# Performance work log

Measured on AMD Instinct MI355X. Metric: run time of the kernel, lower is better.

The kernel has to match this reference:

```python
import jax, jax.numpy as jnp
import numpy as np

N = 100000   # nodes
E = 1600000  # edges (avg degree 16)
D = 128      # in_features == out_features
THETA = 0.25  # hardcoded in the original forward (overwrites log(lamda/l+1))


def setup_inputs() -> dict:
    key = jax.random.key(0)
    k0, k1, k2, k3, k4, k5, k6 = jax.random.split(key, 7)
    stdv = 1.0 / np.sqrt(D)
    return {
        "input": jax.random.normal(k0, (N, D), dtype=jnp.float32),
        "edge_src": jax.random.randint(k1, (E,), 0, N),
        "edge_dst": jax.random.randint(k2, (E,), 0, N),
        "edge_val": jax.random.uniform(k3, (E,), dtype=jnp.float32),
        "h0": jax.random.normal(k4, (N, D), dtype=jnp.float32),
        "weight": jax.random.uniform(k5, (D, D), dtype=jnp.float32, minval=-stdv, maxval=stdv),
        "alpha": jnp.full((1,), 0.4, dtype=jnp.float32),
        "lamda": 1,
        "l": 4,
    }


def reference(input, edge_src, edge_dst, edge_val, h0, weight, alpha, lamda, l):
    # hi = spmm(adj, input): gather source node features, scale by edge weight,
    # segment-sum into destination rows.  [E, D] intermediate -> [N, D]
    hi = jax.ops.segment_sum(input[edge_src] * edge_val[:, None], edge_dst, num_segments=N)
    # original uses alpha.data (detached): sigmoid(alpha)/2
    a = jax.lax.stop_gradient(jax.nn.sigmoid(alpha) / 2.0)  # [1], broadcasts
    # variant=False: support == r == alpha-blend of aggregated and initial features
    support = (1.0 - a) * hi + a * h0
    # theta-scaled dense matmul epilogue + identity-mapping blend
    output = THETA * (support @ weight) + (1.0 - THETA) * support
    # residual=True
    return output + input
```

## Files before the change

kernel.cpp:

```cpp
#include <hip/hip_runtime.h>
#include <hip/hip_bf16.h>

#define DFEAT 128
#define THETA 0.25f
#define SRC_MASK 0xFFFFF
#define DLOW_SH 20
#define SLOWF (1 << 30)
#define SCAP 6144

typedef __attribute__((ext_vector_type(8))) short short8;
typedef __attribute__((ext_vector_type(4))) float f32x4;
typedef __attribute__((ext_vector_type(2))) int i32x2;

__device__ inline unsigned short bf16_bits(float x) {
    __hip_bfloat16 h = __float2bfloat16(x);
    return *reinterpret_cast<unsigned short*>(&h);
}
__device__ inline unsigned pk_bf16(float x, float y) {
    return (unsigned)bf16_bits(x) | ((unsigned)bf16_bits(y) << 16);
}
__device__ inline void fma8(float* A, const uint4 x, float v) {
    A[0] = fmaf(v, __uint_as_float(x.x << 16),         A[0]);
    A[1] = fmaf(v, __uint_as_float(x.x & 0xffff0000u), A[1]);
    A[2] = fmaf(v, __uint_as_float(x.y << 16),         A[2]);
    A[3] = fmaf(v, __uint_as_float(x.y & 0xffff0000u), A[3]);
    A[4] = fmaf(v, __uint_as_float(x.z << 16),         A[4]);
    A[5] = fmaf(v, __uint_as_float(x.z & 0xffff0000u), A[5]);
    A[6] = fmaf(v, __uint_as_float(x.w << 16),         A[6]);
    A[7] = fmaf(v, __uint_as_float(x.w & 0xffff0000u), A[7]);
}

__global__ __launch_bounds__(256) void k_cvt(const float* __restrict__ in,
                                             uint4* __restrict__ o, int n8) {
    int i = blockIdx.x * blockDim.x + threadIdx.x;
    if (i >= n8) return;
    float4 a = reinterpret_cast<const float4*>(in)[(size_t)i * 2];
    float4 b = reinterpret_cast<const float4*>(in)[(size_t)i * 2 + 1];
    uint4 r;
    r.x = pk_bf16(a.x, a.y);
    r.y = pk_bf16(a.z, a.w);
    r.z = pk_bf16(b.x, b.y);
    r.w = pk_bf16(b.z, b.w);
    o[i] = r;
}

__global__ __launch_bounds__(256) void k_wprep(const float* __restrict__ W,
                                               unsigned short* __restrict__ wp) {
    int item = blockIdx.x * blockDim.x + threadIdx.x;
    if (item >= 16 * DFEAT) return;
    int kg = item >> 7;
    int n  = item & 127;
    unsigned pk4[4];
    #pragma unroll
    for (int jj = 0; jj < 4; ++jj) {
        int k0 = kg * 8 + jj * 2;
        float w0 = THETA * W[(size_t)k0 * DFEAT + n];
        float w1 = THETA * W[(size_t)(k0 + 1) * DFEAT + n];
        if (k0 == n)     w0 += 1.0f - THETA;
        if (k0 + 1 == n) w1 += 1.0f - THETA;
        pk4[jj] = pk_bf16(w0, w1);
    }
    uint4 v = make_uint4(pk4[0], pk4[1], pk4[2], pk4[3]);
    int slot = kg ^ (n & 7);
    *reinterpret_cast<uint4*>(&wp[n * DFEAT + slot * 8]) = v;
}

__global__ __launch_bounds__(512) void k_bhist(const int* __restrict__ edst,
                                               int* __restrict__ bcnt, int E) {
    __shared__ int h[512];
    int t = threadIdx.x;
    h[t] = 0;
    __syncthreads();
    int e0 = blockIdx.x * 4096;
    #pragma unroll
    for (int k = 0; k < 8; ++k) {
        int e = e0 + t + k * 512;
        if (e < E) atomicAdd(&h[edst[e] >> 8], 1);
    }
    __syncthreads();
    if (h[t]) atomicAdd(&bcnt[t], h[t]);
}

__global__ __launch_bounds__(512) void k_bscan(const int* __restrict__ bcnt,
                                               int* __restrict__ bbase,
                                               int* __restrict__ tail,
                                               int* __restrict__ rowptr,
                                               int NBUCK, int N, int E) {
    __shared__ int buf[512];
    int t = threadIdx.x;
    buf[t] = (t < NBUCK) ? bcnt[t] : 0;
    __syncthreads();
    for (int off = 1; off < 512; off <<= 1) {
        int y = (t >= off) ? buf[t - off] : 0;
        __syncthreads();
        buf[t] += y;
        __syncthreads();
    }
    if (t < NBUCK) {
        int base = t ? buf[t - 1] : 0;
        bbase[t] = base;
        tail[t]  = base;
    }
    if (t == 0) { bbase[NBUCK] = E; rowptr[N] = E; }
}

__global__ __launch_bounds__(512) void k_bpart(
    const int* __restrict__ esrc, const int* __restrict__ edst,
    const float* __restrict__ eval_, int* __restrict__ tail,
    int2* __restrict__ csr, int E)
{
    __shared__ int histB[512];
    __shared__ int offsB[512];
    __shared__ int gbase[512];
    __shared__ unsigned short bkOf[4096];
    __shared__ int2 stage[4096];

    int t  = threadIdx.x;
    int e0 = blockIdx.x * 4096;
    int szb = min(4096, E - e0);

    histB[t] = 0;
    __syncthreads();

    int myb[8], myr[8];
    int2 mye[8];
    #pragma unroll
    for (int k = 0; k < 8; ++k) {
        int e = e0 + t + k * 512;
        myb[k] = -1;
        if (e < E) {
            int d = edst[e];
            int b = d >> 8;
            mye[k] = make_int2(esrc[e] | ((d & 255) << DLOW_SH),
                               __float_as_int(eval_[e]));
            myb[k] = b;
            myr[k] = atomicAdd(&histB[b], 1);
        }
    }
    __syncthreads();

    offsB[t] = histB[t];
    __syncthreads();
    for (int off = 1; off < 512; off <<= 1) {
        int y = (t >= off) ? offsB[t - off] : 0;
        __syncthreads();
        offsB[t] += y;
        __syncthreads();
    }
    if (histB[t] > 0) gbase[t] = atomicAdd(&tail[t], histB[t]);
    __syncthreads();

    #pragma unroll
    for (int k = 0; k < 8; ++k) {
        if (myb[k] >= 0) {
            int exb = myb[k] ? offsB[myb[k] - 1] : 0;
            int x = exb + myr[k];
            stage[x] = mye[k];
            bkOf[x]  = (unsigned short)myb[k];
        }
    }
    __syncthreads();

    for (int j = t; j < szb; j += 512) {
        int b   = bkOf[j];
        int exb = b ? offsB[b - 1] : 0;
        csr[gbase[b] + (j - exb)] = stage[j];
    }
}

__global__ __launch_bounds__(512) void k_bsort(const int* __restrict__ bbase,
                                               int2* __restrict__ csr,
                                               int* __restrict__ rowptr, int N)
{
    __shared__ int2 stage[SCAP];
    __shared__ int2 stage2[SCAP];
    __shared__ int cntN[256];
    __shared__ int offsN[256];
    __shared__ int curN[256];

    int b  = blockIdx.x;
    int lo = bbase[b], hi = bbase[b + 1];
    int sz = hi - lo;
    int t  = threadIdx.x;
    int node0 = b << 8;

    if (sz > SCAP) {
        if (t < 256) { int n = node0 + t; if (n < N) rowptr[n] = lo | SLOWF; }
        return;
    }

    if (t < 256) cntN[t] = 0;
    for (int j = t; j < sz; j += 512) stage[j] = csr[lo + j];
    __syncthreads();
    for (int j = t; j < sz; j += 512)
        atomicAdd(&cntN[(stage[j].x >> DLOW_SH) & 255], 1);
    __syncthreads();

    if (t < 256) offsN[t] = cntN[t];
    __syncthreads();
    for (int off = 1; off < 256; off <<= 1) {
        int y = (t >= off && t < 256) ? offsN[t - off] : 0;
        __syncthreads();
        if (t < 256) offsN[t] += y;
        __syncthreads();
    }
    if (t < 256) {
        int ex = t ? offsN[t - 1] : 0;
        curN[t] = ex;
        int n = node0 + t;
        if (n < N) rowptr[n] = lo + ex;
    }
    __syncthreads();

    for (int j = t; j < sz; j += 512) {
        int n = (stage[j].x >> DLOW_SH) & 255;
        int pos = atomicAdd(&curN[n], 1);
        stage2[pos] = stage[j];
    }
    __syncthreads();
    for (int j = t; j < sz; j += 512) csr[lo + j] = stage2[j];
}

__global__ __launch_bounds__(256) void k_fused4(
    const unsigned short* __restrict__ in16, const int2* __restrict__ csr,
    const int* __restrict__ rowptr, const float* __restrict__ h0,
    const float* __restrict__ input, const unsigned short* __restrict__ wp,
    const float* __restrict__ alpha, float* __restrict__ out, int N)
{
    __shared__ unsigned short At[16 * DFEAT];

    const int wv   = threadIdx.x >> 6;
    const int lane = threadIdx.x & 63;
    const int ng   = lane >> 4;
    const int s    = lane & 15;

    const int row0 = blockIdx.x * 16;
    const int r    = wv * 4 + ng;
    const int node = row0 + r;

    const float a   = 0.5f / (1.0f + __expf(-alpha[0]));
    const float oma = 1.0f - a;

    float A[8] = {0.f, 0.f, 0.f, 0.f, 0.f, 0.f, 0.f, 0.f};

    if (node < N) {
        int rp = rowptr[node];
        int beg, end;
        if (rp & SLOWF) {
            beg = rp & ~SLOWF;
            int nn = min((((node >> 8) + 1) << 8), N);
            end = rowptr[nn] & ~SLOWF;
        } else {
            beg = rp;
            end = rowptr[node + 1] & ~SLOWF;
        }
        const int dlow = node & 255;

        for (int e = beg; e < end; e += 8) {
            i32x2 p[8];
            uint4 x[8];
            float v[8];
            #pragma unroll
            for (int i = 0; i < 8; ++i) {
                int idx = (e + i < end) ? (e + i) : beg;
                p[i] = __builtin_nontemporal_load(
                    reinterpret_cast<const i32x2*>(&csr[idx]));
            }
            #pragma unroll
            for (int i = 0; i < 8; ++i) {
                x[i] = *reinterpret_cast<const uint4*>(
                    &in16[(size_t)(p[i].x & SRC_MASK) * DFEAT + s * 8]);
                bool ok = (e + i < end) && (((p[i].x >> DLOW_SH) & 255) == dlow);
                v[i] = ok ? __int_as_float(p[i].y) : 0.f;
            }
            #pragma unroll
            for (int i = 0; i < 8; ++i) fma8(A, x[i], v[i]);
        }

        size_t gb = (size_t)node * DFEAT + s * 8;
        f32x4 h0a = __builtin_nontemporal_load(
            reinterpret_cast<const f32x4*>(&h0[gb]));
        f32x4 h0b = __builtin_nontemporal_load(
            reinterpret_cast<const f32x4*>(&h0[gb + 4]));
        float b0 = oma * A[0] + a * h0a.x;
        float b1 = oma * A[1] + a * h0a.y;
        float b2 = oma * A[2] + a * h0a.z;
        float b3 = oma * A[3] + a * h0a.w;
        float b4 = oma * A[4] + a * h0b.x;
        float b5 = oma * A[5] + a * h0b.y;
        float b6 = oma * A[6] + a * h0b.z;
        float b7 = oma * A[7] + a * h0b.w;
        uint4 pk;
        pk.x = pk_bf16(b0, b1);
        pk.y = pk_bf16(b2, b3);
        pk.z = pk_bf16(b4, b5);
        pk.w = pk_bf16(b6, b7);
        *reinterpret_cast<uint4*>(&At[r * DFEAT + ((s ^ (r & 7)) << 3)]) = pk;
    }
    __syncthreads();

    const int m  = lane & 15;
    const int kb = lane >> 4;
    const int n1 = wv * 32 + m;
    const int n2 = n1 + 16;

    short8 bw1[4], bw2[4];
    #pragma unroll
    for (int kk = 0; kk < 4; ++kk) {
        int w = kk * 4 + kb;
        bw1[kk] = *reinterpret_cast<const short8*>(
            &wp[n1 * DFEAT + ((w ^ (n1 & 7)) << 3)]);
        bw2[kk] = *reinterpret_cast<const short8*>(
            &wp[n2 * DFEAT + ((w ^ (n2 & 7)) << 3)]);
    }

    f32x4 acc0 = {0.f, 0.f, 0.f, 0.f};
    f32x4 acc1 = {0.f, 0.f, 0.f, 0.f};
    #pragma unroll
    for (int kk = 0; kk < 4; ++kk) {
        short8 af = *reinterpret_cast<const short8*>(
            &At[m * DFEAT + (((kk * 4 + kb) ^ (m & 7)) << 3)]);
        acc0 = __builtin_amdgcn_mfma_f32_16x16x32_bf16(af, bw1[kk], acc0, 0, 0, 0);
        acc1 = __builtin_amdgcn_mfma_f32_16x16x32_bf16(af, bw2[kk], acc1, 0, 0, 0);
    }

    #pragma unroll
    for (int q = 0; q < 4; ++q) {
        int row = row0 + kb * 4 + q;
        if (row < N) {
            size_t gi = (size_t)row * DFEAT + n1;
            float r0 = __builtin_nontemporal_load(&input[gi]);
            float r1 = __builtin_nontemporal_load(&input[gi + 16]);
            __builtin_nontemporal_store(acc0[q] + r0, &out[gi]);
            __builtin_nontemporal_store(acc1[q] + r1, &out[gi + 16]);
        }
    }
}

__global__ void k_hist(const int* __restrict__ edst, int* __restrict__ cnt, int E) {
    int i = blockIdx.x * blockDim.x + threadIdx.x;
    int e4 = i * 4;
    if (e4 + 4 <= E) {
        int4 d = *reinterpret_cast<const int4*>(&edst[e4]);
        atomicAdd(&cnt[d.x], 1);
        atomicAdd(&cnt[d.y], 1);
        atomicAdd(&cnt[d.z], 1);
        atomicAdd(&cnt[d.w], 1);
    } else {
        for (int e = e4; e < E; ++e) atomicAdd(&cnt[edst[e]], 1);
    }
}

__global__ void k_scanA(const int* __restrict__ cnt, int* __restrict__ part, int N) {
    __shared__ int s[256];
    int i = blockIdx.x * 256 + threadIdx.x;
    s[threadIdx.x] = (i < N) ? cnt[i] : 0;
    __syncthreads();
    for (int off = 128; off > 0; off >>= 1) {
        if (threadIdx.x < off) s[threadIdx.x] += s[threadIdx.x + off];
        __syncthreads();
    }
    if (threadIdx.x == 0) part[blockIdx.x] = s[0];
}

__global__ void k_scanB(int* __restrict__ part, int* __restrict__ rowptr, int B, int N) {
    __shared__ int buf[1024];
    int t = threadIdx.x;
    buf[t] = (t < B) ? part[t] : 0;
    __syncthreads();
    for (int off = 1; off < 1024; off <<= 1) {
        int y = (t >= off) ? buf[t - off] : 0;
        __syncthreads();
        buf[t] += y;
        __syncthreads();
    }
    if (t < B) part[t] = (t == 0) ? 0 : buf[t - 1];
    if (t == B - 1) rowptr[N] = buf[t];
}

__global__ void k_scanC(const int* __restrict__ cnt, const int* __restrict__ part,
                        int* __restrict__ rowptr, int N) {
    __shared__ int buf[256];
    int t = threadIdx.x;
    int i = blockIdx.x * 256 + t;
    buf[t] = (i < N) ? cnt[i] : 0;
    __syncthreads();
    for (int off = 1; off < 256; off <<= 1) {
        int y = (t >= off) ? buf[t - off] : 0;
        __syncthreads();
        buf[t] += y;
        __syncthreads();
    }
    if (i < N) rowptr[i] = part[blockIdx.x] + ((t == 0) ? 0 : buf[t - 1]);
}

__global__ void k_slot(const int* __restrict__ esrc, const int* __restrict__ edst,
                       const float* __restrict__ eval_, const int* __restrict__ rowptr,
                       int* __restrict__ cnt, int2* __restrict__ csr, int E) {
    int i = blockIdx.x * blockDim.x + threadIdx.x;
    int e4 = i * 4;
    if (e4 + 4 <= E) {
        int4   s = *reinterpret_cast<const int4*>(&esrc[e4]);
        int4   d = *reinterpret_cast<const int4*>(&edst[e4]);
        float4 v = *reinterpret_cast<const float4*>(&eval_[e4]);
        int r;
        r = atomicSub(&cnt[d.x], 1); csr[rowptr[d.x] + r - 1] = make_int2(s.x, __float_as_int(v.x));
        r = atomicSub(&cnt[d.y], 1); csr[rowptr[d.y] + r - 1] = make_int2(s.y, __float_as_int(v.y));
        r = atomicSub(&cnt[d.z], 1); csr[rowptr[d.z] + r - 1] = make_int2(s.z, __float_as_int(v.z));
        r = atomicSub(&cnt[d.w], 1); csr[rowptr[d.w] + r - 1] = make_int2(s.w, __float_as_int(v.w));
    } else {
        for (int e = e4; e < E; ++e) {
            int d = edst[e];
            int r = atomicSub(&cnt[d], 1);
            csr[rowptr[d] + r - 1] = make_int2(esrc[e], __float_as_int(eval_[e]));
        }
    }
}

__global__ __launch_bounds__(256) void k_gather(
    const float* __restrict__ input, const int2* __restrict__ csr,
    const int* __restrict__ rowptr, const float* __restrict__ h0,
    const float* __restrict__ alpha, float* __restrict__ out, int N)
{
    int w    = (int)(((long long)blockIdx.x * blockDim.x + threadIdx.x) >> 6);
    int lane = threadIdx.x & 63;
    if (w >= N) return;
    int beg = rowptr[w], end = rowptr[w + 1];
    float ax = 0.f, ay = 0.f, bx = 0.f, by = 0.f;
    int i = beg;
    for (; i + 2 <= end; i += 2) {
        int2 p0 = csr[i], p1 = csr[i + 1];
        float2 x0 = *(const float2*)&input[(size_t)p0.x * DFEAT + lane * 2];
        float2 x1 = *(const float2*)&input[(size_t)p1.x * DFEAT + lane * 2];
        float v0 = __int_as_float(p0.y), v1 = __int_as_float(p1.y);
        ax = fmaf(v0, x0.x, ax); ay = fmaf(v0, x0.y, ay);
        bx = fmaf(v1, x1.x, bx); by = fmaf(v1, x1.y, by);
    }
    if (i < end) {
        int2 p = csr[i];
        float2 x = *(const float2*)&input[(size_t)p.x * DFEAT + lane * 2];
        float v = __int_as_float(p.y);
        ax = fmaf(v, x.x, ax); ay = fmaf(v, x.y, ay);
    }
    float hx = ax + bx, hy = ay + by;
    float a   = 0.5f / (1.0f + __expf(-alpha[0]));
    float oma = 1.0f - a;
    float2 h0v = *(const float2*)&h0[(size_t)w * DFEAT + lane * 2];
    float2 sv;
    sv.x = oma * hx + a * h0v.x;
    sv.y = oma * hy + a * h0v.y;
    *(float2*)&out[(size_t)w * DFEAT + lane * 2] = sv;
}

__global__ __launch_bounds__(256) void gcn_scatter(
    const float* __restrict__ input, const int* __restrict__ esrc,
    const int* __restrict__ edst, const float* __restrict__ eval_,
    float* __restrict__ hi, int E)
{
    long long t = (long long)blockIdx.x * blockDim.x + threadIdx.x;
    int e = (int)(t >> 6);
    if (e >= E) return;
    int lane = (int)(t & 63);
    int s = esrc[e]; int d = edst[e]; float v = eval_[e];
    const float2 x = *reinterpret_cast<const float2*>(&input[(size_t)s * DFEAT + lane * 2]);
    float* p = &hi[(size_t)d * DFEAT + lane * 2];
    unsafeAtomicAdd(p,     x.x * v);
    unsafeAtomicAdd(p + 1, x.y * v);
}

template <bool BLEND>
__global__ __launch_bounds__(256) void gcn_epilogue(
    float* __restrict__ out, const float* __restrict__ h0,
    const float* __restrict__ inp, const float* __restrict__ W,
    const float* __restrict__ alpha, int N)
{
    __shared__ __hip_bfloat16 Wl[DFEAT * DFEAT];
    __shared__ float4 S4[16][DFEAT / 4];

    const float a   = 0.5f / (1.0f + __expf(-alpha[0]));
    const float oma = 1.0f - a;

    for (int i = threadIdx.x; i < DFEAT * DFEAT; i += 256) {
        int k = i >> 7, j = i & 127;
        float w = W[i] * THETA;
        if (k == j) w += 1.0f - THETA;
        Wl[i] = __float2bfloat16(w);
    }

    const int j  = threadIdx.x & 127;
    const int rg = threadIdx.x >> 7;

    for (int base = blockIdx.x * 16; base < N; base += gridDim.x * 16) {
        const int rows = min(16, N - base);
        __syncthreads();
        for (int i = threadIdx.x; i < rows * 32; i += 256) {
            int r = i >> 5, c = i & 31;
            size_t gph = (size_t)(base + r) * (DFEAT / 4) + c;
            float4 hv = reinterpret_cast<const float4*>(out)[gph];
            float4 sv;
            if (BLEND) {
                float4 h0v = reinterpret_cast<const float4*>(h0)[gph];
                sv.x = oma * hv.x + a * h0v.x;
                sv.y = oma * hv.y + a * h0v.y;
                sv.z = oma * hv.z + a * h0v.z;
                sv.w = oma * hv.w + a * h0v.w;
            } else {
                sv = hv;
            }
            S4[r][c] = sv;
        }
        __syncthreads();

        float acc[8];
        #pragma unroll
        for (int r = 0; r < 8; r++) acc[r] = 0.0f;
        for (int k = 0; k < DFEAT; k += 4) {
            float w0 = __bfloat162float(Wl[(k + 0) * DFEAT + j]);
            float w1 = __bfloat162float(Wl[(k + 1) * DFEAT + j]);
            float w2 = __bfloat162float(Wl[(k + 2) * DFEAT + j]);
            float w3 = __bfloat162float(Wl[(k + 3) * DFEAT + j]);
            #pragma unroll
            for (int r = 0; r < 8; r++) {
                float4 s4 = S4[rg * 8 + r][k >> 2];
                acc[r] = fmaf(s4.x, w0, acc[r]);
                acc[r] = fmaf(s4.y, w1, acc[r]);
                acc[r] = fmaf(s4.z, w2, acc[r]);
                acc[r] = fmaf(s4.w, w3, acc[r]);
            }
        }
        #pragma unroll
        for (int r = 0; r < 8; r++) {
            int rr = rg * 8 + r;
            if (rr < rows) {
                size_t gph = (size_t)(base + rr) * DFEAT + j;
                out[gph] = acc[r] + inp[gph];
            }
        }
    }
}

extern "C" void kernel_launch(void* const* d_in, const int* in_sizes, int n_in,
                              void* d_out, int out_size, void* d_ws, size_t ws_size,
                              hipStream_t stream) {
    const float* input = (const float*)d_in[0];
    const int*   esrc  = (const int*)  d_in[1];
    const int*   edst  = (const int*)  d_in[2];
    const float* eval_ = (const float*)d_in[3];
    const float* h0    = (const float*)d_in[4];
    const float* W     = (const float*)d_in[5];
    const float* alpha = (const float*)d_in[6];

    const int N = in_sizes[0] / DFEAT;
    const int E = in_sizes[1];
    float* out = (float*)d_out;
    const int B = (N + 255) / 256;

    size_t bA_in16   = 0;
    size_t bA_csr    = (bA_in16 + (size_t)N * DFEAT * 2 + 15) & ~(size_t)15;
    size_t bA_rowptr = bA_csr + (size_t)E * 8;
    size_t bA_bkt    = bA_rowptr + (size_t)(N + 1) * 4;
    size_t bA_wp     = (bA_bkt + (size_t)N * 4 + 15) & ~(size_t)15;
    size_t needA     = bA_wp + (size_t)DFEAT * DFEAT * 2;

    size_t o_rowptr = 0;
    size_t o_cnt    = o_rowptr + (size_t)(N + 1);
    size_t o_part   = o_cnt + (size_t)N;
    size_t o_csr    = (o_part + 1024 + 1) & ~(size_t)1;
    size_t needB    = o_csr * 4 + (size_t)E * 8;

    const int NBUCK = (N + 255) >> 8;

    if (ws_size >= needA && N <= 131072 && N >= 1600) {
        unsigned short* in16 = (unsigned short*)((char*)d_ws + bA_in16);
        int2* csr    = (int2*)((char*)d_ws + bA_csr);
        int*  rowptr = (int*) ((char*)d_ws + bA_rowptr);
        int*  bcnt   = (int*) ((char*)d_ws + bA_bkt);
        int*  bbase  = bcnt + 512;
        int*  tail   = bbase + 513;
        unsigned short* wp = (unsigned short*)((char*)d_ws + bA_wp);

        int n8     = N * DFEAT / 8;
        int ntiles = (N + 15) / 16;
        int nEB    = (E + 4095) / 4096;

        hipMemsetAsync(bcnt, 0, 512 * sizeof(int), stream);
        k_cvt  <<<dim3((n8 + 255) / 256), dim3(256), 0, stream>>>(input, (uint4*)in16, n8);
        k_wprep<<<dim3(8),                dim3(256), 0, stream>>>(W, wp);
        k_bhist<<<dim3(nEB),              dim3(512), 0, stream>>>(edst, bcnt, E);
        k_bscan<<<dim3(1),                dim3(512), 0, stream>>>(bcnt, bbase, tail,
                                                                  rowptr, NBUCK, N, E);
        k_bpart<<<dim3(nEB),              dim3(512), 0, stream>>>(esrc, edst, eval_,
                                                                  tail, csr, E);
        k_bsort<<<dim3(NBUCK),            dim3(512), 0, stream>>>(bbase, csr, rowptr, N);
        k_fused4<<<dim3(ntiles),          dim3(256), 0, stream>>>(in16, csr, rowptr,
                                                                  h0, input, wp, alpha,
                                                                  out, N);
    } else if (ws_size >= needB && B <= 1024) {
        int*  rowptr = (int*)d_ws + o_rowptr;
        int*  cnt    = (int*)d_ws + o_cnt;
        int*  part   = (int*)d_ws + o_part;
        int2* csr    = (int2*)((int*)d_ws + o_csr);
        int E4 = (E + 3) / 4;

        hipMemsetAsync(cnt, 0, (size_t)N * sizeof(int), stream);
        k_hist <<<dim3((E4 + 255) / 256), dim3(256), 0, stream>>>(edst, cnt, E);
        k_scanA<<<dim3(B),               dim3(256), 0, stream>>>(cnt, part, N);
        k_scanB<<<dim3(1),               dim3(1024), 0, stream>>>(part, rowptr, B, N);
        k_scanC<<<dim3(B),               dim3(256), 0, stream>>>(cnt, part, rowptr, N);
        k_slot <<<dim3((E4 + 255) / 256), dim3(256), 0, stream>>>(esrc, edst, eval_,
                                                                  rowptr, cnt, csr, E);
        k_gather<<<dim3((N + 3) / 4),    dim3(256), 0, stream>>>(input, csr, rowptr,
                                                                 h0, alpha, out, N);
        gcn_epilogue<false><<<dim3(2048), dim3(256), 0, stream>>>(out, h0, input, W,
                                                                  alpha, N);
    } else {
        hipMemsetAsync(out, 0, (size_t)N * DFEAT * sizeof(float), stream);
        long long threads = (long long)E * 64;
        unsigned  nblk    = (unsigned)((threads + 255) / 256);
        gcn_scatter<<<dim3(nblk), dim3(256), 0, stream>>>(input, esrc, edst, eval_, out, E);
        gcn_epilogue<true><<<dim3(2048), dim3(256), 0, stream>>>(out, h0, input, W,
                                                                 alpha, N);
    }
}
```

Baseline: 177.3 us.

## Fold memset and weight prep into other kernels, drop bsort staging, unroll gather 16

```diff
diff --git a/kernel.cpp b/kernel.cpp
--- a/kernel.cpp
+++ b/kernel.cpp
@@ -31,7 +31,12 @@
 }
 
 __global__ __launch_bounds__(256) void k_cvt(const float* __restrict__ in,
-                                             uint4* __restrict__ o, int n8) {
+                                             uint4* __restrict__ o, int n8,
+                                             int* __restrict__ bcnt) {
+    if (blockIdx.x == 0) {
+        bcnt[threadIdx.x] = 0;
+        bcnt[threadIdx.x + 256] = 0;
+    }
     int i = blockIdx.x * blockDim.x + threadIdx.x;
     if (i >= n8) return;
     float4 a = reinterpret_cast<const float4*>(in)[(size_t)i * 2];
@@ -44,27 +49,6 @@
     o[i] = r;
 }
 
-__global__ __launch_bounds__(256) void k_wprep(const float* __restrict__ W,
-                                               unsigned short* __restrict__ wp) {
-    int item = blockIdx.x * blockDim.x + threadIdx.x;
-    if (item >= 16 * DFEAT) return;
-    int kg = item >> 7;
-    int n  = item & 127;
-    unsigned pk4[4];
-    #pragma unroll
-    for (int jj = 0; jj < 4; ++jj) {
-        int k0 = kg * 8 + jj * 2;
-        float w0 = THETA * W[(size_t)k0 * DFEAT + n];
-        float w1 = THETA * W[(size_t)(k0 + 1) * DFEAT + n];
-        if (k0 == n)     w0 += 1.0f - THETA;
-        if (k0 + 1 == n) w1 += 1.0f - THETA;
-        pk4[jj] = pk_bf16(w0, w1);
-    }
-    uint4 v = make_uint4(pk4[0], pk4[1], pk4[2], pk4[3]);
-    int slot = kg ^ (n & 7);
-    *reinterpret_cast<uint4*>(&wp[n * DFEAT + slot * 8]) = v;
-}
-
 __global__ __launch_bounds__(512) void k_bhist(const int* __restrict__ edst,
                                                int* __restrict__ bcnt, int E) {
     __shared__ int h[512];
@@ -81,27 +65,48 @@
     if (h[t]) atomicAdd(&bcnt[t], h[t]);
 }
 
-__global__ __launch_bounds__(512) void k_bscan(const int* __restrict__ bcnt,
-                                               int* __restrict__ bbase,
-                                               int* __restrict__ tail,
-                                               int* __restrict__ rowptr,
-                                               int NBUCK, int N, int E) {
-    __shared__ int buf[512];
-    int t = threadIdx.x;
-    buf[t] = (t < NBUCK) ? bcnt[t] : 0;
-    __syncthreads();
-    for (int off = 1; off < 512; off <<= 1) {
-        int y = (t >= off) ? buf[t - off] : 0;
-        __syncthreads();
-        buf[t] += y;
-        __syncthreads();
-    }
-    if (t < NBUCK) {
-        int base = t ? buf[t - 1] : 0;
-        bbase[t] = base;
-        tail[t]  = base;
-    }
-    if (t == 0) { bbase[NBUCK] = E; rowptr[N] = E; }
+__global__ __launch_bounds__(512) void k_bscan_wprep(
+    const int* __restrict__ bcnt, int* __restrict__ bbase,
+    int* __restrict__ tail, int* __restrict__ rowptr,
+    int NBUCK, int N, int E,
+    const float* __restrict__ W, unsigned short* __restrict__ wp)
+{
+    if (blockIdx.x == 0) {
+        __shared__ int buf[512];
+        int t = threadIdx.x;
+        buf[t] = (t < NBUCK) ? bcnt[t] : 0;
+        __syncthreads();
+        for (int off = 1; off < 512; off <<= 1) {
+            int y = (t >= off) ? buf[t - off] : 0;
+            __syncthreads();
+            buf[t] += y;
+            __syncthreads();
+        }
+        if (t < NBUCK) {
+            int base = t ? buf[t - 1] : 0;
+            bbase[t] = base;
+            tail[t]  = base;
+        }
+        if (t == 0) { bbase[NBUCK] = E; rowptr[N] = E; }
+    } else {
+        int item = (blockIdx.x - 1) * 512 + threadIdx.x;
+        if (item >= 16 * DFEAT) return;
+        int kg = item >> 7;
+        int n  = item & 127;
+        unsigned pk4[4];
+        #pragma unroll
+        for (int jj = 0; jj < 4; ++jj) {
+            int k0 = kg * 8 + jj * 2;
+            float w0 = THETA * W[(size_t)k0 * DFEAT + n];
+            float w1 = THETA * W[(size_t)(k0 + 1) * DFEAT + n];
+            if (k0 == n)     w0 += 1.0f - THETA;
+            if (k0 + 1 == n) w1 += 1.0f - THETA;
+            pk4[jj] = pk_bf16(w0, w1);
+        }
+        uint4 v = make_uint4(pk4[0], pk4[1], pk4[2], pk4[3]);
+        int slot = kg ^ (n & 7);
+        *reinterpret_cast<uint4*>(&wp[n * DFEAT + slot * 8]) = v;
+    }
 }
 
 __global__ __launch_bounds__(512) void k_bpart(
@@ -173,7 +178,6 @@
                                                int* __restrict__ rowptr, int N)
 {
     __shared__ int2 stage[SCAP];
-    __shared__ int2 stage2[SCAP];
     __shared__ int cntN[256];
     __shared__ int offsN[256];
     __shared__ int curN[256];
@@ -215,13 +219,11 @@
     for (int j = t; j < sz; j += 512) {
         int n = (stage[j].x >> DLOW_SH) & 255;
         int pos = atomicAdd(&curN[n], 1);
-        stage2[pos] = stage[j];
-    }
-    __syncthreads();
-    for (int j = t; j < sz; j += 512) csr[lo + j] = stage2[j];
-}
-
-__global__ __launch_bounds__(256) void k_fused4(
+        csr[lo + pos] = stage[j];
+    }
+}
+
+__global__ __launch_bounds__(256) void k_fused5(
     const unsigned short* __restrict__ in16, const int2* __restrict__ csr,
     const int* __restrict__ rowptr, const float* __restrict__ h0,
     const float* __restrict__ input, const unsigned short* __restrict__ wp,
@@ -256,25 +258,25 @@
         }
         const int dlow = node & 255;
 
-        for (int e = beg; e < end; e += 8) {
-            i32x2 p[8];
-            uint4 x[8];
-            float v[8];
+        for (int e = beg; e < end; e += 16) {
+            i32x2 p[16];
+            uint4 x[16];
+            float v[16];
             #pragma unroll
-            for (int i = 0; i < 8; ++i) {
+            for (int i = 0; i < 16; ++i) {
                 int idx = (e + i < end) ? (e + i) : beg;
                 p[i] = __builtin_nontemporal_load(
                     reinterpret_cast<const i32x2*>(&csr[idx]));
             }
             #pragma unroll
-            for (int i = 0; i < 8; ++i) {
+            for (int i = 0; i < 16; ++i) {
                 x[i] = *reinterpret_cast<const uint4*>(
                     &in16[(size_t)(p[i].x & SRC_MASK) * DFEAT + s * 8]);
                 bool ok = (e + i < end) && (((p[i].x >> DLOW_SH) & 255) == dlow);
                 v[i] = ok ? __int_as_float(p[i].y) : 0.f;
             }
             #pragma unroll
-            for (int i = 0; i < 8; ++i) fma8(A, x[i], v[i]);
+            for (int i = 0; i < 16; ++i) fma8(A, x[i], v[i]);
         }
 
         size_t gb = (size_t)node * DFEAT + s * 8;
@@ -583,16 +585,16 @@
         int ntiles = (N + 15) / 16;
         int nEB    = (E + 4095) / 4096;
 
-        hipMemsetAsync(bcnt, 0, 512 * sizeof(int), stream);
-        k_cvt  <<<dim3((n8 + 255) / 256), dim3(256), 0, stream>>>(input, (uint4*)in16, n8);
-        k_wprep<<<dim3(8),                dim3(256), 0, stream>>>(W, wp);
+        k_cvt  <<<dim3((n8 + 255) / 256), dim3(256), 0, stream>>>(input, (uint4*)in16,
+                                                                  n8, bcnt);
         k_bhist<<<dim3(nEB),              dim3(512), 0, stream>>>(edst, bcnt, E);
-        k_bscan<<<dim3(1),                dim3(512), 0, stream>>>(bcnt, bbase, tail,
-                                                                  rowptr, NBUCK, N, E);
+        k_bscan_wprep<<<dim3(5),          dim3(512), 0, stream>>>(bcnt, bbase, tail,
+                                                                  rowptr, NBUCK, N, E,
+                                                                  W, wp);
         k_bpart<<<dim3(nEB),              dim3(512), 0, stream>>>(esrc, edst, eval_,
                                                                   tail, csr, E);
         k_bsort<<<dim3(NBUCK),            dim3(512), 0, stream>>>(bbase, csr, rowptr, N);
-        k_fused4<<<dim3(ntiles),          dim3(256), 0, stream>>>(in16, csr, rowptr,
+        k_fused5<<<dim3(ntiles),          dim3(256), 0, stream>>>(in16, csr, rowptr,
                                                                   h0, input, wp, alpha,
                                                                   out, N);
     } else if (ws_size >= needB && B <= 1024) {
```

New measurement: 171.8 us. 1.03x faster.
